# Kernel optimization log

Measured on AMD Instinct MI355X. Metric: run time of the kernel, lower is better.

## Reference

```python
import jax, jax.numpy as jnp
import numpy as np

DIM = 3072
DIM_HEAD = 128
HEADS = 16
KV_DIM = 2048
INNER = DIM_HEAD * HEADS  # 2048


def layernorm(x, g, b, eps=1e-5):
    mu = jnp.mean(x, axis=-1, keepdims=True)
    var = jnp.mean((x - mu) ** 2, axis=-1, keepdims=True)
    return (x - mu) * jax.lax.rsqrt(var + eps) * g + b


def setup_inputs() -> dict:
    key = jax.random.key(0)
    ks = jax.random.split(key, 6)
    b, n1, n2 = 2, 4096, 1024
    x = jax.random.normal(ks[0], (b, n1, KV_DIM), dtype=jnp.float32)
    latents = jax.random.normal(ks[1], (b, n2, DIM), dtype=jnp.float32)
    # Linear weights stored [in, out] (torch stores [out, in]; math is x @ W)
    Wq = jax.random.normal(ks[2], (DIM, INNER), dtype=jnp.float32) * 0.02
    Wkv = jax.random.normal(ks[3], (KV_DIM, 2 * INNER), dtype=jnp.float32) * 0.02
    Wout = jax.random.normal(ks[4], (INNER, DIM), dtype=jnp.float32) * 0.02
    ln1_g = jnp.ones((KV_DIM,), jnp.float32)
    ln1_b = jnp.zeros((KV_DIM,), jnp.float32)
    ln2_g = jnp.ones((DIM,), jnp.float32)
    ln2_b = jnp.zeros((DIM,), jnp.float32)
    return {"x": x, "latents": latents, "ln1_g": ln1_g, "ln1_b": ln1_b,
            "ln2_g": ln2_g, "ln2_b": ln2_b, "Wq": Wq, "Wkv": Wkv, "Wout": Wout}


def reference(x, latents, ln1_g, ln1_b, ln2_g, ln2_b, Wq, Wkv, Wout):
    b, n2, _ = latents.shape
    xn = layernorm(x, ln1_g, ln1_b)          # (b, n1, kv_dim)
    ln = layernorm(latents, ln2_g, ln2_b)    # (b, n2, dim)
    q = ln @ Wq                               # (b, n2, inner)
    kv = xn @ Wkv                             # (b, n1, 2*inner)
    k, v = jnp.split(kv, 2, axis=-1)
    # (b, seq, h*d) -> (b, h, seq, d)
    def heads(t):
        bs, L, _ = t.shape
        return t.reshape(bs, L, HEADS, DIM_HEAD).transpose(0, 2, 1, 3)
    q, k, v = heads(q), heads(k), heads(v)
    scale = 1.0 / np.sqrt(np.sqrt(DIM_HEAD)).astype(np.float32)
    logits = jnp.einsum('bhqd,bhkd->bhqk', q * scale, k * scale)
    w = jax.nn.softmax(logits.astype(jnp.float32), axis=-1).astype(logits.dtype)
    out = jnp.einsum('bhqk,bhkd->bhqd', w, v)  # (b, h, n2, d)
    out = out.transpose(0, 2, 1, 3).reshape(b, n2, INNER)
    return out @ Wout
```

## Files before the change

### kernel.cpp

```cpp
#include <hip/hip_runtime.h>
#include <stdint.h>

typedef unsigned short u16;
typedef unsigned int u32;
typedef __attribute__((ext_vector_type(4))) float f32x4;
typedef __attribute__((ext_vector_type(8))) __bf16 bf16x8;

#define N1T 4096
#define N2T 1024
#define DIMT 3072
#define KVD 2048
#define INN 2048
#define NH 16
#define DH 128

__device__ __forceinline__ u16 f2bf(float f) {
  u32 u = __builtin_bit_cast(u32, f);
  u = (u + 0x7fffu + ((u >> 16) & 1u)) >> 16;
  return (u16)u;
}

__device__ __forceinline__ float exp2_fast(float x) {
  return __builtin_amdgcn_exp2f(x);
}

__device__ __forceinline__ u32 cvtpk(float lo, float hi) {
  u32 r;
  asm volatile("v_cvt_pk_bf16_f32 %0, %1, %2" : "=v"(r) : "v"(lo), "v"(hi));
  return r;
}

typedef __attribute__((address_space(1))) void gvoid_t;
typedef __attribute__((address_space(3))) void lvoid_t;

__device__ __forceinline__ void gload16(const void* g, void* l) {
  __builtin_amdgcn_global_load_lds((gvoid_t*)g, (lvoid_t*)l, 16, 0, 0);
}

template<int NV>
__global__ __launch_bounds__(256) void ln_cast_kernel(
    const float* __restrict__ X, const float* __restrict__ G,
    const float* __restrict__ B, u16* __restrict__ out) {
  const int D = NV * 1024;
  const int t = threadIdx.x;
  const size_t row = blockIdx.x;
  const float4* xr = (const float4*)(X + row * D);
  float4 v[NV];
  float s = 0.f, ss = 0.f;
#pragma unroll
  for (int i = 0; i < NV; ++i) {
    v[i] = xr[i * 256 + t];
    s += v[i].x + v[i].y + v[i].z + v[i].w;
    ss += v[i].x * v[i].x + v[i].y * v[i].y + v[i].z * v[i].z + v[i].w * v[i].w;
  }
#pragma unroll
  for (int off = 32; off; off >>= 1) {
    s += __shfl_xor(s, off);
    ss += __shfl_xor(ss, off);
  }
  __shared__ float red[2][4];
  const int wave = t >> 6, lane = t & 63;
  if (lane == 0) { red[0][wave] = s; red[1][wave] = ss; }
  __syncthreads();
  s = red[0][0] + red[0][1] + red[0][2] + red[0][3];
  ss = red[1][0] + red[1][1] + red[1][2] + red[1][3];
  const float mu = s / D;
  const float rstd = rsqrtf(ss / D - mu * mu + 1e-5f);
  u16* orow = out + row * D;
#pragma unroll
  for (int i = 0; i < NV; ++i) {
    const int idx = (i * 256 + t) * 4;
    float4 g4 = *(const float4*)(G + idx);
    float4 b4 = *(const float4*)(B + idx);
    union { ushort4 v4; u16 h[4]; } pk;
    pk.h[0] = f2bf((v[i].x - mu) * rstd * g4.x + b4.x);
    pk.h[1] = f2bf((v[i].y - mu) * rstd * g4.y + b4.y);
    pk.h[2] = f2bf((v[i].z - mu) * rstd * g4.z + b4.z);
    pk.h[3] = f2bf((v[i].w - mu) * rstd * g4.w + b4.w);
    *(ushort4*)(orow + idx) = pk.v4;
  }
}

__global__ __launch_bounds__(256) void tcast_kernel(
    const float* __restrict__ W, u16* __restrict__ WT, int K, int N) {
  __shared__ __align__(16) u16 tile[64][72];
  const int t = threadIdx.x;
  const int k0 = blockIdx.x * 64, n0 = blockIdx.y * 64;
#pragma unroll
  for (int i = 0; i < 4; ++i) {
    int idx = i * 256 + t;
    int r = idx >> 4, c = (idx & 15) << 2;
    float4 v = *(const float4*)(W + (size_t)(k0 + r) * N + n0 + c);
    union { ushort4 v4; u16 h[4]; } pk;
    pk.h[0] = f2bf(v.x); pk.h[1] = f2bf(v.y);
    pk.h[2] = f2bf(v.z); pk.h[3] = f2bf(v.w);
    *(ushort4*)&tile[r][c] = pk.v4;
  }
  __syncthreads();
#pragma unroll
  for (int j = 0; j < 2; ++j) {
    int cid = j * 256 + t;
    int nr = cid >> 3, kc = (cid & 7) << 3;
    union { uint4 v4; u16 h[8]; } pk;
#pragma unroll
    for (int jj = 0; jj < 8; ++jj) pk.h[jj] = tile[kc + jj][nr];
    *(uint4*)(WT + (size_t)(n0 + nr) * K + k0 + kc) = pk.v4;
  }
}

template<int BF16OUT>
__global__ __launch_bounds__(256) void gemm_bt_kernel(
    const u16* __restrict__ A, size_t Az,
    const u16* __restrict__ Bt, size_t Btz,
    void* __restrict__ Cv, size_t Cz,
    int M, int N, int K, float scale) {
  __shared__ __align__(16) u16 As[128 * 64];
  __shared__ __align__(16) u16 Bs[128 * 64];
  A += (size_t)blockIdx.z * Az;
  Bt += (size_t)blockIdx.z * Btz;
  const int t = threadIdx.x, lane = t & 63, wave = t >> 6;
  const int m0 = blockIdx.x * 128, n0 = blockIdx.y * 128;
  const int wr = (wave >> 1) * 64, wc = (wave & 1) * 64;
  const int fr = lane & 15, fk = (lane >> 4) * 8;
  f32x4 acc[4][4];
#pragma unroll
  for (int i = 0; i < 4; ++i)
#pragma unroll
    for (int j = 0; j < 4; ++j)
#pragma unroll
      for (int r = 0; r < 4; ++r) acc[i][j][r] = 0.f;
  const int srow = t >> 3;
  const int scb = (t & 7) * 16;
  const int nk = K >> 6;
  for (int kt = 0; kt < nk; ++kt) {
    const char* Ab = (const char*)(A + (size_t)kt * 64);
    const char* Bb = (const char*)(Bt + (size_t)kt * 64);
#pragma unroll
    for (int r = 0; r < 4; ++r) {
      int row = srow + r * 32;
      gload16(Ab + (size_t)(m0 + row) * K * 2 + scb, (char*)As + t * 16 + r * 4096);
      gload16(Bb + (size_t)(n0 + row) * K * 2 + scb, (char*)Bs + t * 16 + r * 4096);
    }
    __syncthreads();
#pragma unroll
    for (int kk = 0; kk < 2; ++kk) {
      bf16x8 af[4], bfr[4];
#pragma unroll
      for (int i = 0; i < 4; ++i)
        af[i] = *(const bf16x8*)&As[(wr + i * 16 + fr) * 64 + kk * 32 + fk];
#pragma unroll
      for (int j = 0; j < 4; ++j)
        bfr[j] = *(const bf16x8*)&Bs[(wc + j * 16 + fr) * 64 + kk * 32 + fk];
#pragma unroll
      for (int i = 0; i < 4; ++i)
#pragma unroll
        for (int j = 0; j < 4; ++j)
          acc[i][j] = __builtin_amdgcn_mfma_f32_16x16x32_bf16(af[i], bfr[j], acc[i][j], 0, 0, 0);
    }
    __syncthreads();
  }
  const int cr = (lane >> 4) * 4, cc = lane & 15;
#pragma unroll
  for (int i = 0; i < 4; ++i)
#pragma unroll
    for (int j = 0; j < 4; ++j) {
      const int row = m0 + wr + i * 16 + cr;
      const int col = n0 + wc + j * 16 + cc;
      if (BF16OUT) {
        u16* C = (u16*)Cv + (size_t)blockIdx.z * Cz;
#pragma unroll
        for (int r = 0; r < 4; ++r) C[(size_t)(row + r) * N + col] = f2bf(acc[i][j][r] * scale);
      } else {
        float* C = (float*)Cv + (size_t)blockIdx.z * Cz;
#pragma unroll
        for (int r = 0; r < 4; ++r) C[(size_t)(row + r) * N + col] = acc[i][j][r];
      }
    }
}

__device__ __forceinline__ void stage_region(const u16* __restrict__ G, int ldk,
                                             int rowbase, int colbase,
                                             u16* lds, int t) {
  const int srow = t >> 2, sc = t & 3;
  const int swz = (srow >> 1) & 3;
#pragma unroll
  for (int r = 0; r < 2; ++r) {
    int row = r * 128 + srow;
    gload16(G + (size_t)(rowbase + row) * ldk + colbase + (sc ^ swz) * 8,
            (char*)lds + t * 16 + r * 8192);
  }
}

#define GPHASE(MSUB, KK, STAGE_STMT, RELOAD_B, VM0)                               \
  {                                                                               \
    STAGE_STMT;                                                                   \
    const u16* Aarr = (KK) ? A1s : A0s;                                           \
    _Pragma("unroll")                                                             \
    for (int fi = 0; fi < 4; ++fi) {                                              \
      int rowa = RM + (MSUB) * 64 + fi * 16 + fr;                                 \
      af[fi] = *(const bf16x8*)((const char*)Aarr + rowa * 64 +                   \
                                ((q ^ ((rowa >> 1) & 3)) * 16));                  \
    }                                                                             \
    if (RELOAD_B) {                                                               \
      const u16* Barr = (KK) ? B1s : B0s;                                         \
      _Pragma("unroll")                                                           \
      for (int j = 0; j < 4; ++j) {                                               \
        int rowb = RN + j * 16 + fr;                                              \
        bf[j] = *(const bf16x8*)((const char*)Barr + rowb * 64 +                  \
                                 ((q ^ ((rowb >> 1) & 3)) * 16));                 \
      }                                                                           \
    }                                                                             \
    if (VM0) { asm volatile("s_waitcnt vmcnt(0)" ::: "memory"); }                 \
    else     { asm volatile("s_waitcnt vmcnt(2)" ::: "memory"); }                 \
    __builtin_amdgcn_s_barrier();                                                 \
    asm volatile("s_waitcnt lgkmcnt(0)" ::: "memory");                            \
    __builtin_amdgcn_sched_barrier(0);                                            \
    __builtin_amdgcn_s_setprio(1);                                                \
    _Pragma("unroll")                                                             \
    for (int fi = 0; fi < 4; ++fi)                                                \
      _Pragma("unroll")                                                           \
      for (int j = 0; j < 4; ++j)                                                 \
        acc[(MSUB) * 4 + fi][j] = __builtin_amdgcn_mfma_f32_16x16x32_bf16(        \
            af[fi], bf[j], acc[(MSUB) * 4 + fi][j], 0, 0, 0);                     \
    __builtin_amdgcn_s_setprio(0);                                                \
    __builtin_amdgcn_s_barrier();                                                 \
  }

template<int BF16OUT>
__global__ __launch_bounds__(512) void gemm256_kernel(
    const u16* __restrict__ A, size_t Az,
    const u16* __restrict__ Bt, size_t Btz,
    void* __restrict__ Cv, size_t Cz,
    int M, int N, int K, float scale) {
  __shared__ __align__(16) u16 A0s[256 * 32];
  __shared__ __align__(16) u16 A1s[256 * 32];
  __shared__ __align__(16) u16 B0s[256 * 32];
  __shared__ __align__(16) u16 B1s[256 * 32];
  A += (size_t)blockIdx.z * Az;
  Bt += (size_t)blockIdx.z * Btz;
  const int t = threadIdx.x, lane = t & 63, wave = t >> 6;
  const int m0 = blockIdx.x * 256, n0 = blockIdx.y * 256;
  const int RM = (wave >> 2) * 128, RN = (wave & 3) * 64;
  const int fr = lane & 15, q = lane >> 4;
  f32x4 acc[8][4];
#pragma unroll
  for (int i = 0; i < 8; ++i)
#pragma unroll
    for (int j = 0; j < 4; ++j)
#pragma unroll
      for (int r = 0; r < 4; ++r) acc[i][j][r] = 0.f;

  stage_region(Bt, K, n0, 0, B0s, t);
  stage_region(A, K, m0, 0, A0s, t);
  stage_region(Bt, K, n0, 32, B1s, t);
  asm volatile("s_waitcnt vmcnt(0)" ::: "memory");
  __builtin_amdgcn_s_barrier();

  const int nk = K >> 6;
#pragma unroll 1
  for (int kt = 0; kt < nk; ++kt) {
    const bool last = (kt == nk - 1);
    bf16x8 af[4], bf[4];
    GPHASE(0, 0, stage_region(A, K, m0, kt * 64 + 32, A1s, t), true, false)
    GPHASE(1, 0, if (!last) stage_region(Bt, K, n0, (kt + 1) * 64, B0s, t), false, last)
    GPHASE(1, 1, if (!last) stage_region(A, K, m0, (kt + 1) * 64, A0s, t), true, last)
    GPHASE(0, 1, if (!last) stage_region(Bt, K, n0, (kt + 1) * 64 + 32, B1s, t), false, last)
  }

  const int cr = (lane >> 4) * 4, cc = lane & 15;
#pragma unroll
  for (int i = 0; i < 8; ++i)
#pragma unroll
    for (int j = 0; j < 4; ++j) {
      const int row = m0 + RM + i * 16 + cr;
      const int col = n0 + RN + j * 16 + cc;
      if (BF16OUT) {
        u16* C = (u16*)Cv + (size_t)blockIdx.z * Cz;
#pragma unroll
        for (int r = 0; r < 4; ++r) C[(size_t)(row + r) * N + col] = f2bf(acc[i][j][r] * scale);
      } else {
        float* C = (float*)Cv + (size_t)blockIdx.z * Cz;
#pragma unroll
        for (int r = 0; r < 4; ++r) C[(size_t)(row + r) * N + col] = acc[i][j][r];
      }
    }
}

#define KVB 128
__device__ __forceinline__ int swz4(int row) {
  return ((row & 15) ^ (((row >> 4) & 1) << 2)) << 4;
}

__device__ __forceinline__ void stage_kv(const u16* Kbase, const u16* Vbase,
                                         int kv0, char* ks, char* vs, int t) {
  const int col = (t & 15) * 16;
#pragma unroll
  for (int r = 0; r < 4; ++r) {
    int row = (t >> 4) + r * 32;
    gload16((const char*)(Kbase + (size_t)(kv0 + row) * INN) + (col ^ swz4(row)),
            ks + t * 16 + r * 8192);
  }
#pragma unroll
  for (int r = 0; r < 4; ++r) {
    int row = (t >> 4) + r * 32;
    gload16((const char*)(Vbase + (size_t)row * N1T + kv0) + (col ^ swz4(row)),
            vs + t * 16 + r * 8192);
  }
}

__global__ __launch_bounds__(512, 2) void attn_kernel(
    const u16* __restrict__ Q, const u16* __restrict__ Kb,
    const u16* __restrict__ Vt, float* __restrict__ Opart,
    float* __restrict__ ml) {
  __shared__ __align__(16) u16 Ks[2][KVB * 128];
  __shared__ __align__(16) u16 Vs[2][128 * KVB];
  const int t = threadIdx.x, lane = t & 63, wave = t >> 6;
  const int bid = blockIdx.x;
  const int xcd = bid & 7, idx = bid >> 3;
  const int bh = (xcd << 2) | (idx >> 3);
  const int sub = idx & 7;
  const int qt = sub >> 1, half = sub & 1;
  const int b = bh >> 4, h = bh & 15;
  const int q0 = qt * 256 + wave * 32;
  const int fr = lane & 15, quad = lane >> 4;
  const int fk = quad * 8;
  const int frp = fr + (fr & 12);

  bf16x8 qf0[4], qf1[4];
  {
    const u16* qr0 = Q + (size_t)(b * N2T + q0 + fr) * INN + h * DH;
    const u16* qr1 = Q + (size_t)(b * N2T + q0 + 16 + fr) * INN + h * DH;
#pragma unroll
    for (int c = 0; c < 4; ++c) {
      qf0[c] = *(const bf16x8*)(qr0 + c * 32 + fk);
      qf1[c] = *(const bf16x8*)(qr1 + c * 32 + fk);
    }
  }

  float m_run[2] = {-1e30f, -1e30f}, l_run[2] = {0.f, 0.f};
  f32x4 oT[2][8];
#pragma unroll
  for (int f = 0; f < 2; ++f)
#pragma unroll
    for (int i = 0; i < 8; ++i)
#pragma unroll
      for (int r = 0; r < 4; ++r) oT[f][i][r] = 0.f;

  const u16* Kbase = Kb + (size_t)(b * N1T) * INN + h * DH;
  const u16* Vbase = Vt + ((size_t)b * INN + h * DH) * N1T;
  const int kvb = half * 2048;

  const int NT = 2048 / KVB;
  int cur = 0;
  stage_kv(Kbase, Vbase, kvb, (char*)&Ks[0][0], (char*)&Vs[0][0], t);
  for (int tile = 0; tile < NT; ++tile) {
    if (tile + 1 < NT) {
      stage_kv(Kbase, Vbase, kvb + (tile + 1) * KVB, (char*)&Ks[cur ^ 1][0],
               (char*)&Vs[cur ^ 1][0], t);
      asm volatile("s_waitcnt vmcnt(8)" ::: "memory");
    } else {
      asm volatile("s_waitcnt vmcnt(0)" ::: "memory");
    }
    __builtin_amdgcn_s_barrier();
    __builtin_amdgcn_sched_barrier(0);
    const char* KsC = (const char*)&Ks[cur][0];
    const char* VsC = (const char*)&Vs[cur][0];

    f32x4 sT[2][8];
    __builtin_amdgcn_s_setprio(1);
#pragma unroll
    for (int ni = 0; ni < 8; ++ni) {
#pragma unroll
      for (int r = 0; r < 4; ++r) { sT[0][ni][r] = 0.f; sT[1][ni][r] = 0.f; }
      const int rowa = (ni >> 1) * 32 + (ni & 1) * 4 + frp;
      const int sz = swz4(rowa);
#pragma unroll
      for (int c = 0; c < 4; ++c) {
        bf16x8 kf = *(const bf16x8*)(KsC + rowa * 256 + ((c * 64 + quad * 16) ^ sz));
        sT[0][ni] = __builtin_amdgcn_mfma_f32_16x16x32_bf16(kf, qf0[c], sT[0][ni], 0, 0, 0);
        sT[1][ni] = __builtin_amdgcn_mfma_f32_16x16x32_bf16(kf, qf1[c], sT[1][ni], 0, 0, 0);
      }
    }
    __builtin_amdgcn_s_setprio(0);
    union { u32 w[4]; bf16x8 v; } pa[2][4];
#pragma unroll
    for (int f = 0; f < 2; ++f) {
      float mt = sT[f][0][0];
#pragma unroll
      for (int ni = 0; ni < 8; ++ni)
#pragma unroll
        for (int r = 0; r < 4; ++r) mt = fmaxf(mt, sT[f][ni][r]);
      mt = fmaxf(mt, __shfl_xor(mt, 16));
      mt = fmaxf(mt, __shfl_xor(mt, 32));
      if (!__all(mt <= m_run[f] + 10.f)) {
        float mnew = fmaxf(m_run[f], mt);
        float alpha = exp2_fast(m_run[f] - mnew);
        m_run[f] = mnew;
        l_run[f] *= alpha;
#pragma unroll
        for (int i = 0; i < 8; ++i)
#pragma unroll
          for (int r = 0; r < 4; ++r) oT[f][i][r] *= alpha;
      }
      float lt = 0.f;
#pragma unroll
      for (int ni = 0; ni < 8; ++ni)
#pragma unroll
        for (int r = 0; r < 4; ++r) {
          sT[f][ni][r] = exp2_fast(sT[f][ni][r] - m_run[f]);
          lt += sT[f][ni][r];
        }
      lt += __shfl_xor(lt, 16);
      lt += __shfl_xor(lt, 32);
      l_run[f] += lt;
#pragma unroll
      for (int kk = 0; kk < 4; ++kk) {
        pa[f][kk].w[0] = cvtpk(sT[f][kk * 2][0], sT[f][kk * 2][1]);
        pa[f][kk].w[1] = cvtpk(sT[f][kk * 2][2], sT[f][kk * 2][3]);
        pa[f][kk].w[2] = cvtpk(sT[f][kk * 2 + 1][0], sT[f][kk * 2 + 1][1]);
        pa[f][kk].w[3] = cvtpk(sT[f][kk * 2 + 1][2], sT[f][kk * 2 + 1][3]);
      }
    }
    __builtin_amdgcn_s_setprio(1);
#pragma unroll
    for (int ni2 = 0; ni2 < 8; ++ni2) {
      const int rowv = ni2 * 16 + fr;
      const int sz = swz4(rowv);
#pragma unroll
      for (int kk = 0; kk < 4; ++kk) {
        bf16x8 vf = *(const bf16x8*)(VsC + rowv * 256 + ((kk * 64 + quad * 16) ^ sz));
        oT[0][ni2] = __builtin_amdgcn_mfma_f32_16x16x32_bf16(vf, pa[0][kk].v, oT[0][ni2], 0, 0, 0);
        oT[1][ni2] = __builtin_amdgcn_mfma_f32_16x16x32_bf16(vf, pa[1][kk].v, oT[1][ni2], 0, 0, 0);
      }
    }
    __builtin_amdgcn_s_setprio(0);
    __builtin_amdgcn_sched_barrier(0);
    __builtin_amdgcn_s_barrier();
    cur ^= 1;
  }
#pragma unroll
  for (int f = 0; f < 2; ++f) {
    const size_t row = (size_t)(b * N2T + q0 + f * 16 + fr) * 16 + h;
    float* op = Opart + ((size_t)half * 32768 + row) * 128 + quad * 4;
#pragma unroll
    for (int ni2 = 0; ni2 < 8; ++ni2) {
      float4 v4 = {oT[f][ni2][0], oT[f][ni2][1], oT[f][ni2][2], oT[f][ni2][3]};
      *(float4*)(op + ni2 * 16) = v4;
    }
    if (quad == 0) {
      float2 v2 = {m_run[f], l_run[f]};
      *(float2*)(ml + ((size_t)half * 32768 + row) * 2) = v2;
    }
  }
}

__global__ __launch_bounds__(256) void combine2_kernel(
    const float* __restrict__ Opart, const float* __restrict__ ml,
    u16* __restrict__ ab) {
  const int tid = blockIdx.x * 256 + threadIdx.x;
  const int row = tid >> 5;
  const int c = tid & 31;
  float2 ml1 = *(const float2*)(ml + (size_t)row * 2);
  float2 ml2 = *(const float2*)(ml + ((size_t)32768 + row) * 2);
  float m = fmaxf(ml1.x, ml2.x);
  float w1 = exp2_fast(ml1.x - m), w2 = exp2_fast(ml2.x - m);
  float inv = 1.0f / (w1 * ml1.y + w2 * ml2.y);
  float4 o1 = *(const float4*)(Opart + (size_t)row * 128 + c * 4);
  float4 o2 = *(const float4*)(Opart + ((size_t)32768 + row) * 128 + c * 4);
  union { ushort4 v4; u16 hh[4]; } pk;
  pk.hh[0] = f2bf((w1 * o1.x + w2 * o2.x) * inv);
  pk.hh[1] = f2bf((w1 * o1.y + w2 * o2.y) * inv);
  pk.hh[2] = f2bf((w1 * o1.z + w2 * o2.z) * inv);
  pk.hh[3] = f2bf((w1 * o1.w + w2 * o2.w) * inv);
  *(ushort4*)(ab + (size_t)(row >> 4) * 2048 + (row & 15) * 128 + c * 4) = pk.v4;
}

extern "C" void kernel_launch(void* const* d_in, const int* in_sizes, int n_in,
                              void* d_out, int out_size, void* d_ws, size_t ws_size,
                              hipStream_t stream) {
  const float* x = (const float*)d_in[0];
  const float* latents = (const float*)d_in[1];
  const float* ln1g = (const float*)d_in[2];
  const float* ln1b = (const float*)d_in[3];
  const float* ln2g = (const float*)d_in[4];
  const float* ln2b = (const float*)d_in[5];
  const float* Wq = (const float*)d_in[6];
  const float* Wkv = (const float*)d_in[7];
  const float* Wout = (const float*)d_in[8];

  char* w = (char*)d_ws;
  u16* xn = (u16*)w;   w += (size_t)8192 * 2048 * 2;
  u16* lnb = (u16*)w;  w += (size_t)2048 * 3072 * 2;
  u16* WqT = (u16*)w;  w += (size_t)2048 * 3072 * 2;
  u16* WkvT = (u16*)w; w += (size_t)4096 * 2048 * 2;
  u16* WoT = (u16*)w;  w += (size_t)3072 * 2048 * 2;
  u16* qb = (u16*)w;   w += (size_t)2048 * 2048 * 2;
  u16* kb = (u16*)w;   w += (size_t)8192 * 2048 * 2;
  u16* vtb = (u16*)w;  w += (size_t)2 * 2048 * 4096 * 2;
  u16* ab = (u16*)w;   w += (size_t)2048 * 2048 * 2;
  float* opart = (float*)d_ws;
  float* mlbuf = (float*)((char*)d_ws + 33554432);

  dim3 blk(256);
  tcast_kernel<<<dim3(48, 32), blk, 0, stream>>>(Wq, WqT, 3072, 2048);
  tcast_kernel<<<dim3(32, 64), blk, 0, stream>>>(Wkv, WkvT, 2048, 4096);
  tcast_kernel<<<dim3(32, 48), blk, 0, stream>>>(Wout, WoT, 2048, 3072);
  ln_cast_kernel<2><<<8192, blk, 0, stream>>>(x, ln1g, ln1b, xn);
  ln_cast_kernel<3><<<2048, blk, 0, stream>>>(latents, ln2g, ln2b, lnb);

  const float scale = 0.29730177875068026f;
  const float qscale = scale * 1.4426950408889634f;
  gemm_bt_kernel<1><<<dim3(16, 16, 1), blk, 0, stream>>>(
      lnb, 0, WqT, 0, qb, 0, 2048, 2048, 3072, qscale);
  gemm256_kernel<1><<<dim3(32, 8, 1), dim3(512), 0, stream>>>(
      xn, 0, WkvT, 0, kb, 0, 8192, 2048, 2048, scale);
  gemm256_kernel<1><<<dim3(8, 16, 2), dim3(512), 0, stream>>>(
      WkvT + (size_t)2048 * 2048, 0, xn, (size_t)4096 * 2048,
      vtb, (size_t)2048 * 4096, 2048, 4096, 2048, 1.0f);
  attn_kernel<<<dim3(256), dim3(512), 0, stream>>>(qb, kb, vtb, opart, mlbuf);
  combine2_kernel<<<dim3(4096), blk, 0, stream>>>(opart, mlbuf, ab);
  gemm_bt_kernel<0><<<dim3(16, 24, 1), blk, 0, stream>>>(
      ab, 0, WoT, 0, d_out, 0, 2048, 3072, 2048, 1.0f);
}
```

Baseline: 396.7 us.

## Double-buffer GEMM LDS tiles and drop trailing per-phase barrier

The 256x256 GEMM kernel's LDS staging buffers are doubled so the next k-tile is loaded into a separate buffer while the current one is consumed. Loads are issued two regions at a time with vmcnt(4) waits, and the trailing barrier after each MFMA phase is removed. The aim is to give global loads more time in flight and cut synchronisation per k-step. In exchange, LDS use doubles to 128KB per block, which may limit occupancy, and removing barriers adds a risk of read/write races on the buffers.

Result: slower. 419.3 us (+5.7%).

```diff
diff --git a/kernel.cpp b/kernel.cpp
--- a/kernel.cpp
+++ b/kernel.cpp
@@ -191,10 +191,10 @@
   }
 }
 
-#define GPHASE(MSUB, KK, STAGE_STMT, RELOAD_B, VM0)                               \
+#define GPHASE(MSUB, KK, STAGE_STMT, RELOAD_B, WAIT_STMT)                         \
   {                                                                               \
     STAGE_STMT;                                                                   \
-    const u16* Aarr = (KK) ? A1s : A0s;                                           \
+    const u16* Aarr = (KK) ? &A1s[cb][0] : &A0s[cb][0];                           \
     _Pragma("unroll")                                                             \
     for (int fi = 0; fi < 4; ++fi) {                                              \
       int rowa = RM + (MSUB) * 64 + fi * 16 + fr;                                 \
@@ -202,7 +202,7 @@
                                 ((q ^ ((rowa >> 1) & 3)) * 16));                  \
     }                                                                             \
     if (RELOAD_B) {                                                               \
-      const u16* Barr = (KK) ? B1s : B0s;                                         \
+      const u16* Barr = (KK) ? &B1s[cb][0] : &B0s[cb][0];                         \
       _Pragma("unroll")                                                           \
       for (int j = 0; j < 4; ++j) {                                               \
         int rowb = RN + j * 16 + fr;                                              \
@@ -210,8 +210,7 @@
                                  ((q ^ ((rowb >> 1) & 3)) * 16));                 \
       }                                                                           \
     }                                                                             \
-    if (VM0) { asm volatile("s_waitcnt vmcnt(0)" ::: "memory"); }                 \
-    else     { asm volatile("s_waitcnt vmcnt(2)" ::: "memory"); }                 \
+    WAIT_STMT;                                                                    \
     __builtin_amdgcn_s_barrier();                                                 \
     asm volatile("s_waitcnt lgkmcnt(0)" ::: "memory");                            \
     __builtin_amdgcn_sched_barrier(0);                                            \
@@ -223,8 +222,10 @@
         acc[(MSUB) * 4 + fi][j] = __builtin_amdgcn_mfma_f32_16x16x32_bf16(        \
             af[fi], bf[j], acc[(MSUB) * 4 + fi][j], 0, 0, 0);                     \
     __builtin_amdgcn_s_setprio(0);                                                \
-    __builtin_amdgcn_s_barrier();                                                 \
-  }
+  }
+
+#define VMW4 asm volatile("s_waitcnt vmcnt(4)" ::: "memory")
+#define VMW0 asm volatile("s_waitcnt vmcnt(0)" ::: "memory")
 
 template<int BF16OUT>
 __global__ __launch_bounds__(512) void gemm256_kernel(
@@ -232,10 +233,10 @@
     const u16* __restrict__ Bt, size_t Btz,
     void* __restrict__ Cv, size_t Cz,
     int M, int N, int K, float scale) {
-  __shared__ __align__(16) u16 A0s[256 * 32];
-  __shared__ __align__(16) u16 A1s[256 * 32];
-  __shared__ __align__(16) u16 B0s[256 * 32];
-  __shared__ __align__(16) u16 B1s[256 * 32];
+  __shared__ __align__(16) u16 A0s[2][256 * 32];
+  __shared__ __align__(16) u16 A1s[2][256 * 32];
+  __shared__ __align__(16) u16 B0s[2][256 * 32];
+  __shared__ __align__(16) u16 B1s[2][256 * 32];
   A += (size_t)blockIdx.z * Az;
   Bt += (size_t)blockIdx.z * Btz;
   const int t = threadIdx.x, lane = t & 63, wave = t >> 6;
@@ -250,21 +251,29 @@
 #pragma unroll
       for (int r = 0; r < 4; ++r) acc[i][j][r] = 0.f;
 
-  stage_region(Bt, K, n0, 0, B0s, t);
-  stage_region(A, K, m0, 0, A0s, t);
-  stage_region(Bt, K, n0, 32, B1s, t);
-  asm volatile("s_waitcnt vmcnt(0)" ::: "memory");
+  stage_region(A, K, m0, 0, &A0s[0][0], t);
+  stage_region(Bt, K, n0, 0, &B0s[0][0], t);
+  stage_region(A, K, m0, 32, &A1s[0][0], t);
+  stage_region(Bt, K, n0, 32, &B1s[0][0], t);
+  VMW0;
   __builtin_amdgcn_s_barrier();
 
   const int nk = K >> 6;
 #pragma unroll 1
   for (int kt = 0; kt < nk; ++kt) {
     const bool last = (kt == nk - 1);
+    const int cb = kt & 1, nb = cb ^ 1;
     bf16x8 af[4], bf[4];
-    GPHASE(0, 0, stage_region(A, K, m0, kt * 64 + 32, A1s, t), true, false)
-    GPHASE(1, 0, if (!last) stage_region(Bt, K, n0, (kt + 1) * 64, B0s, t), false, last)
-    GPHASE(1, 1, if (!last) stage_region(A, K, m0, (kt + 1) * 64, A0s, t), true, last)
-    GPHASE(0, 1, if (!last) stage_region(Bt, K, n0, (kt + 1) * 64 + 32, B1s, t), false, last)
+    GPHASE(0, 0,
+           if (!last) { stage_region(A, K, m0, (kt + 1) * 64, &A0s[nb][0], t);
+                        stage_region(Bt, K, n0, (kt + 1) * 64, &B0s[nb][0], t); },
+           true, (void)0)
+    GPHASE(1, 0, (void)0, false, if (last) { VMW0; } else { VMW4; })
+    GPHASE(1, 1,
+           if (!last) { stage_region(A, K, m0, (kt + 1) * 64 + 32, &A1s[nb][0], t);
+                        stage_region(Bt, K, n0, (kt + 1) * 64 + 32, &B1s[nb][0], t); },
+           true, (void)0)
+    GPHASE(0, 1, (void)0, false, if (!last) { VMW4; })
   }
 
   const int cr = (lane >> 4) * 4, cc = lane & 15;
```
